# Performance work log

Hardware: AMD Instinct MI355X
Metric: run time of the kernel (lower is better)

Reference implementation:

```python
import jax, jax.numpy as jnp
import numpy as np

N_NODES = 200000
N_EDGES = 2000000
B = 1024
SEQ = 1000
EMB = 128
VOC = 26  # num_features_xt + 1
BN_EPS = 1e-5


def setup_inputs() -> dict:
    key = jax.random.key(0)
    ks = jax.random.split(key, 40)
    f32 = jnp.float32
    def nrm(k, shp, s=0.05):
        return jax.random.normal(k, shp, dtype=f32) * s
    inp = {}
    inp['x'] = jax.random.normal(ks[0], (N_NODES, 78), dtype=f32)
    inp['edge_index'] = jax.random.randint(ks[1], (2, N_EDGES), 0, N_NODES, dtype=jnp.int32)
    inp['batch'] = jnp.sort(jax.random.randint(ks[2], (N_NODES,), 0, B, dtype=jnp.int32))
    inp['target'] = jax.random.randint(ks[3], (B, SEQ), 0, VOC, dtype=jnp.int32)
    # GIN layer 1 (78 -> 32 -> 32)
    inp['W1a'] = nrm(ks[4], (78, 32)); inp['b1a'] = jnp.zeros((32,), f32)
    inp['W2a'] = nrm(ks[5], (32, 32)); inp['b2a'] = jnp.zeros((32,), f32)
    inp['g1'] = jnp.ones((32,), f32); inp['be1'] = jnp.zeros((32,), f32)
    # GIN layers 2-5 stacked
    inp['Ws1'] = nrm(ks[6], (4, 32, 32)); inp['bs1'] = jnp.zeros((4, 32), f32)
    inp['Ws2'] = nrm(ks[7], (4, 32, 32)); inp['bs2'] = jnp.zeros((4, 32), f32)
    inp['gs'] = jnp.ones((4, 32), f32); inp['bes'] = jnp.zeros((4, 32), f32)
    # drug head
    inp['fc1xd_W'] = nrm(ks[8], (32, 128)); inp['fc1xd_b'] = jnp.zeros((128,), f32)
    # protein branch
    inp['emb'] = nrm(ks[9], (VOC, EMB), 1.0)
    inp['convW'] = nrm(ks[10], (32, SEQ, 8))  # Conv1d(1000, 32, k=8): (O, I, K)
    inp['convb'] = jnp.zeros((32,), f32)
    inp['fcxt_W'] = nrm(ks[11], (32 * 121, 128)); inp['fcxt_b'] = jnp.zeros((128,), f32)
    # joint head
    inp['fc1_W'] = nrm(ks[12], (256, 1024)); inp['fc1_b'] = jnp.zeros((1024,), f32)
    inp['fc2_W'] = nrm(ks[13], (1024, 256)); inp['fc2_b'] = jnp.zeros((256,), f32)
    inp['out_W'] = nrm(ks[14], (256, 1)); inp['out_b'] = jnp.zeros((1,), f32)
    return inp


def _bn(h, g, b):
    m = h.mean(axis=0)
    v = h.var(axis=0)
    return (h - m) * jax.lax.rsqrt(v + BN_EPS) * g + b


def _gin(x, src, dst, W1, b1, W2, b2):
    # GIN aggregation (eps=0): (1+eps)*x + sum_{j->i} x_j, then 2-layer MLP
    agg = jax.ops.segment_sum(x[src], dst, num_segments=x.shape[0]) + x
    return jnp.maximum(agg @ W1 + b1, 0.0) @ W2 + b2


def reference(x, edge_index, batch, target, W1a, b1a, W2a, b2a, g1, be1,
              Ws1, bs1, Ws2, bs2, gs, bes, fc1xd_W, fc1xd_b, emb, convW, convb,
              fcxt_W, fcxt_b, fc1_W, fc1_b, fc2_W, fc2_b, out_W, out_b):
    relu = jax.nn.relu
    src, dst = edge_index[0], edge_index[1]
    h = _bn(relu(_gin(x, src, dst, W1a, b1a, W2a, b2a)), g1, be1)
    for i in range(4):
        h = _bn(relu(_gin(h, src, dst, Ws1[i], bs1[i], Ws2[i], bs2[i])), gs[i], bes[i])
    nb = target.shape[0]
    pooled = jax.ops.segment_sum(h, batch, num_segments=nb)  # [B, 32]
    xd = relu(pooled @ fc1xd_W + fc1xd_b)  # dropout: identity at eval
    # protein branch: embedding [B, 1000, 128] -> Conv1d over C=1000, L=128
    xe = emb[target]
    conv = jax.lax.conv_general_dilated(xe, convW, (1,), 'VALID',
                                        dimension_numbers=('NCH', 'OIH', 'NCH'))
    conv = conv + convb[None, :, None]  # [B, 32, 121]
    xt = conv.reshape(nb, 32 * 121) @ fcxt_W + fcxt_b
    xc = jnp.concatenate([xd, xt], axis=1)
    xc = relu(xc @ fc1_W + fc1_b)
    xc = relu(xc @ fc2_W + fc2_b)
    return xc @ out_W + out_b
```

## Files before the change

### kernel.cpp

```cpp
#include <hip/hip_runtime.h>

#define N_NODES 200000
#define N_EDGES 2000000
#define BATCH   1024
#define SEQ     1000
#define EMBD    128
#define VOC     26
#define BN_EPS  1e-5f
#define NB      128
#define NBUK    1563
#define CAP     2048
#define STG     8192
#define BPT     7



__global__ __launch_bounds__(256, 1) void k_bscatter(const int* __restrict__ ei,
                                                     int* __restrict__ gcnt,
                                                     unsigned int* __restrict__ epk) {
    __shared__ int lcnt[NBUK];
    __shared__ int lpos[NBUK];
    __shared__ int sbase[NBUK];
    __shared__ int ssum[256];
    __shared__ int2 stage[STG];
    int tid = threadIdx.x;
    int e0 = blockIdx.x * STG;
    int m = min(STG, N_EDGES - e0);
    for (int i = tid; i < NBUK; i += 256) lcnt[i] = 0;
    __syncthreads();
    for (int i = tid; i < m; i += 256) {
        int d = ei[N_EDGES + e0 + i];
        atomicAdd(&lcnt[d >> 7], 1);
    }
    __syncthreads();
    int v[BPT]; int s0 = 0; int bb = tid * BPT;
#pragma unroll
    for (int k = 0; k < BPT; k++) {
        int idx = bb + k;
        v[k] = (idx < NBUK) ? lcnt[idx] : 0;
        s0 += v[k];
    }
    ssum[tid] = s0;
    __syncthreads();
    for (int off = 1; off < 256; off <<= 1) {
        int x = (tid >= off) ? ssum[tid - off] : 0;
        __syncthreads();
        ssum[tid] += x;
        __syncthreads();
    }
    int run = ssum[tid] - s0;
#pragma unroll
    for (int k = 0; k < BPT; k++) {
        int idx = bb + k;
        if (idx < NBUK) { lpos[idx] = run; run += v[k]; }
    }
    __syncthreads();
    for (int i = tid; i < NBUK; i += 256) {
        int c = lcnt[i];
        if (c > 0) {
            int gb = atomicAdd(&gcnt[i], c);
            sbase[i] = gb - lpos[i];
        }
    }
    __syncthreads();
    for (int i = tid; i < m; i += 256) {
        int s = ei[e0 + i];
        int d = ei[N_EDGES + e0 + i];
        int p = atomicAdd(&lpos[d >> 7], 1);
        stage[p] = make_int2(s, d);
    }
    __syncthreads();
    for (int i = tid; i < m; i += 256) {
        int2 ed = stage[i];
        int b = ed.y >> 7;
        int slot = sbase[b] + i;
        if (slot < CAP)
            epk[(size_t)b * CAP + slot] = ((unsigned int)ed.x << 8) | (unsigned int)(ed.y & 127);
    }
}

__global__ __launch_bounds__(256, 8) void k_bsort(const int* __restrict__ gcnt,
                                                  unsigned int* __restrict__ epk,
                                                  int* __restrict__ deg) {
    __shared__ unsigned int stg[CAP];
    __shared__ unsigned int srt[CAP];
    __shared__ int cnt[NB];
    __shared__ int pos[NB];
    int b = blockIdx.x, tid = threadIdx.x;
    int fill = min(gcnt[b], CAP);
    unsigned int* slab = epk + (size_t)b * CAP;
    for (int i = tid; i < fill; i += 256) stg[i] = slab[i];
    if (tid < NB) cnt[tid] = 0;
    __syncthreads();
    for (int i = tid; i < fill; i += 256) atomicAdd(&cnt[stg[i] & (NB - 1)], 1);
    __syncthreads();
    if (tid < NB) { pos[tid] = cnt[tid]; deg[b * NB + tid] = cnt[tid]; }
    __syncthreads();
    for (int off = 1; off < NB; off <<= 1) {
        int x = (tid < NB && tid >= off) ? pos[tid - off] : 0;
        __syncthreads();
        if (tid < NB) pos[tid] += x;
        __syncthreads();
    }
    if (tid < NB) cnt[tid] = pos[tid] - cnt[tid];
    __syncthreads();
    for (int i = tid; i < fill; i += 256) {
        int p = atomicAdd(&cnt[stg[i] & (NB - 1)], 1);
        srt[p] = stg[i];
    }
    __syncthreads();
    for (int i = tid; i < fill; i += 256) slab[i] = srt[i];
}


__global__ __launch_bounds__(128) void k_proj78(const float* __restrict__ x,
                                                const float* __restrict__ W,
                                                float* __restrict__ y) {
    __shared__ __align__(16) float xs[128 * 78];
    __shared__ __align__(16) float ws[78 * 32];
    int tid = threadIdx.x;
    int base = blockIdx.x * 128;
    for (int i = tid; i < 78 * 32; i += 128) ws[i] = W[i];
    int cnt = min(128, N_NODES - base);
    for (int i = tid; i < cnt * 78; i += 128) xs[i] = x[(size_t)base * 78 + i];
    __syncthreads();
    int n = base + tid;
    if (tid >= cnt) return;
    float acc[32];
#pragma unroll
    for (int j = 0; j < 32; j++) acc[j] = 0.f;
    const float* xr = &xs[tid * 78];
    for (int c = 0; c < 78; c++) {
        float xv = xr[c];
        const float4* w4 = (const float4*)&ws[c * 32];
#pragma unroll
        for (int j4 = 0; j4 < 8; j4++) {
            float4 w = w4[j4];
            acc[j4 * 4 + 0] += xv * w.x; acc[j4 * 4 + 1] += xv * w.y;
            acc[j4 * 4 + 2] += xv * w.z; acc[j4 * 4 + 3] += xv * w.w;
        }
    }
    float4* yo = (float4*)&y[(size_t)n * 32];
#pragma unroll
    for (int j4 = 0; j4 < 8; j4++)
        yo[j4] = make_float4(acc[j4*4], acc[j4*4+1], acc[j4*4+2], acc[j4*4+3]);
}

template <bool FOLD>
__global__ __launch_bounds__(256, 4) void k_gmlp(const float* __restrict__ hin,
                                                 const int* __restrict__ gcnt,
                                                 const unsigned int* __restrict__ epk,
                                                 const int* __restrict__ deg,
                                                 const float* __restrict__ stats,
                                                 const float* __restrict__ g,
                                                 const float* __restrict__ be,
                                                 const float* __restrict__ W1,
                                                 const float* __restrict__ b1,
                                                 const float* __restrict__ W2,
                                                 const float* __restrict__ b2,
                                                 float* __restrict__ h,
                                                 float* __restrict__ statsOut) {
    __shared__ __align__(16) float ts[NB * 33];
    __shared__ __align__(16) float w2s[1024];
    __shared__ __align__(16) float wc[FOLD ? 1024 : 4];
    __shared__ __align__(16) unsigned int es[CAP];
    __shared__ float as_[FOLD ? 32 : 1], cs_[FOLD ? 32 : 1], cv[FOLD ? 32 : 1];
    __shared__ float b1s[32], b2s[32];
    __shared__ float sp[8][32], sq[8][32];
    int tid = threadIdx.x, base = blockIdx.x * NB;
    for (int i = tid; i < 1024; i += 256) w2s[i] = W2[i];
    if (tid < 32) { b1s[tid] = b1[tid]; b2s[tid] = b2[tid]; }
    if constexpr (FOLD) {
        if (tid < 32) {
            float inv_n = 1.f / (float)N_NODES;
            float m = stats[tid] * inv_n;
            float var = stats[32 + tid] * inv_n - m * m;
            float a = g[tid] * rsqrtf(var + BN_EPS);
            as_[tid] = a;
            cs_[tid] = be[tid] - m * a;
        }
        __syncthreads();
        for (int i = tid; i < 1024; i += 256) wc[i] = as_[i >> 5] * W1[i];
        if (tid < 32) {
            float s = 0.f;
            for (int k = 0; k < 32; k++) s += cs_[k] * W1[k * 32 + tid];
            cv[tid] = s;
        }
    }
    int cnt = min(NB, N_NODES - base);
    int fill = min(gcnt[blockIdx.x], CAP);
    int pfill = (fill + 255) & ~255;
    int dg = 0;
    if (FOLD && tid < cnt) dg = deg[base + tid];
    for (int i = tid; i < fill; i += 256) es[i] = epk[(size_t)blockIdx.x * CAP + i];
    for (int i = fill + tid; i < pfill; i += 256) es[i] = 128u;
    for (int i = tid; i < cnt * 32; i += 256) ts[(i >> 5) * 33 + (i & 31)] = hin[(size_t)base * 32 + i];
    __syncthreads();
    {
        int hw = tid >> 5, c = tid & 31;
        for (int se = hw * 32; se < pfill; se += 256) {
            float rr[32]; unsigned int dpk[8];
#pragma unroll
            for (int k4 = 0; k4 < 8; k4++) {
                unsigned int dp = 0;
#pragma unroll
                for (int q = 0; q < 4; q++) {
                    unsigned int p = es[se + k4 * 4 + q];
                    rr[k4 * 4 + q] = hin[(size_t)(p >> 8) * 32 + c];
                    dp |= (p & 255u) << (8 * q);
                }
                dpk[k4] = dp;
            }
            float acc = rr[0]; int cur = (int)(dpk[0] & 255u);
#pragma unroll
            for (int k = 1; k < 32; k++) {
                int d = (int)((dpk[k >> 2] >> (8 * (k & 3))) & 255u);
                if (d == cur) acc += rr[k];
                else { atomicAdd(&ts[cur * 33 + c], acc); acc = rr[k]; cur = d; }
            }
            if (cur < 128) atomicAdd(&ts[cur * 33 + c], acc);
        }
    }
    __syncthreads();
    float t[32];
    if (tid < cnt) {
        float v[32];
        if constexpr (FOLD) {
            float dgf = (float)(dg + 1);
#pragma unroll
            for (int j = 0; j < 32; j++) v[j] = b1s[j] + dgf * cv[j];
            for (int c = 0; c < 32; c++) {
                float av = ts[tid * 33 + c];
                const float4* w4 = (const float4*)&wc[c * 32];
#pragma unroll
                for (int j4 = 0; j4 < 8; j4++) {
                    float4 w = w4[j4];
                    v[j4*4+0] += av * w.x; v[j4*4+1] += av * w.y;
                    v[j4*4+2] += av * w.z; v[j4*4+3] += av * w.w;
                }
            }
        } else {
#pragma unroll
            for (int c = 0; c < 32; c++) v[c] = ts[tid * 33 + c] + b1s[c];
        }
        float acc[32];
#pragma unroll
        for (int j = 0; j < 32; j++) acc[j] = b2s[j];
        for (int c = 0; c < 32; c++) {
            float zv = fmaxf(v[c], 0.f);
            const float4* w4 = (const float4*)&w2s[c * 32];
#pragma unroll
            for (int j4 = 0; j4 < 8; j4++) {
                float4 w = w4[j4];
                acc[j4*4+0] += zv * w.x; acc[j4*4+1] += zv * w.y;
                acc[j4*4+2] += zv * w.z; acc[j4*4+3] += zv * w.w;
            }
        }
#pragma unroll
        for (int j = 0; j < 32; j++) t[j] = fmaxf(acc[j], 0.f);
    } else {
#pragma unroll
        for (int j = 0; j < 32; j++) t[j] = 0.f;
    }
    __syncthreads();
    if (tid < NB) {
#pragma unroll
        for (int c = 0; c < 32; c++) ts[tid * 33 + c] = t[c];
    }
    __syncthreads();
    {
        int c = tid & 31, gg = tid >> 5;
        float s = 0.f, q = 0.f;
        for (int r = gg * 16; r < gg * 16 + 16; r++) { float vv = ts[r * 33 + c]; s += vv; q += vv * vv; }
        sp[gg][c] = s; sq[gg][c] = q;
    }
    __syncthreads();
    if (tid < 32) {
        float s = 0.f, q = 0.f;
#pragma unroll
        for (int gg = 0; gg < 8; gg++) { s += sp[gg][tid]; q += sq[gg][tid]; }
        atomicAdd(&statsOut[tid], s);
        atomicAdd(&statsOut[32 + tid], q);
    }
    for (int i = tid; i < cnt * 32; i += 256) h[(size_t)base * 32 + i] = ts[(i >> 5) * 33 + (i & 31)];
}

__device__ __forceinline__ int lbound(const int* __restrict__ b, int val) {
    int lo = 0, hi = N_NODES;
    while (lo < hi) { int mid = (lo + hi) >> 1; if (b[mid] < val) lo = mid + 1; else hi = mid; }
    return lo;
}

__global__ __launch_bounds__(256) void k_pool(const float* __restrict__ h,
                                              const int* __restrict__ batch,
                                              const float* __restrict__ stats,
                                              const float* __restrict__ gw,
                                              const float* __restrict__ be,
                                              float* __restrict__ pooled) {
    __shared__ float sp[8][32];
    int g = blockIdx.x;
    int start = lbound(batch, g), end = lbound(batch, g + 1);
    int c = threadIdx.x & 31, gg = threadIdx.x >> 5;
    float acc = 0.f;
    for (int r = start + gg; r < end; r += 8) acc += h[(size_t)r * 32 + c];
    sp[gg][c] = acc;
    __syncthreads();
    if (threadIdx.x < 32) {
        int j = threadIdx.x;
        float s = 0.f;
#pragma unroll
        for (int k = 0; k < 8; k++) s += sp[k][j];
        float inv_n = 1.f / (float)N_NODES;
        float m = stats[j] * inv_n;
        float var = stats[32 + j] * inv_n - m * m;
        float a = gw[j] * rsqrtf(var + BN_EPS);
        float cc = be[j] - m * a;
        pooled[g * 32 + j] = a * s + cc * (float)(end - start);
    }
}

__global__ __launch_bounds__(256) void k_xd(const float* __restrict__ pooled,
                                            const float* __restrict__ W,
                                            const float* __restrict__ b,
                                            float* __restrict__ xc) {
    int t = blockIdx.x * 256 + threadIdx.x;
    int row = t >> 7, col = t & 127;
    if (row >= BATCH) return;
    float acc = b[col];
    for (int k = 0; k < 32; k++) acc += pooled[row * 32 + k] * W[k * 128 + col];
    xc[row * 256 + col] = fmaxf(acc, 0.f);
}


__global__ __launch_bounds__(256) void k_trw(const float* __restrict__ convW,
                                             float* __restrict__ Wt) {
    int t = blockIdx.x * 256 + threadIdx.x;
    if (t >= 32 * SEQ * 8) return;
    int o = t / (SEQ * 8), r = t % (SEQ * 8), i = r >> 3, k = r & 7;
    Wt[i * 256 + o * 8 + k] = convW[t];
}

__global__ __launch_bounds__(256) void k_prot1(const int* __restrict__ target,
                                               const float* __restrict__ Wt,
                                               float* __restrict__ Sg) {
    __shared__ int tv[SEQ];
    __shared__ int pos_[SEQ];
    __shared__ int off_[VOC + 1];
    __shared__ int cur_[VOC];
    int tid = threadIdx.x, b = blockIdx.x;
    for (int i = tid; i < SEQ; i += 256) tv[i] = target[(size_t)b * SEQ + i];
    if (tid < VOC + 1) off_[tid] = 0;
    __syncthreads();
    for (int i = tid; i < SEQ; i += 256) atomicAdd(&off_[tv[i] + 1], 1);
    __syncthreads();
    if (tid == 0) for (int v = 1; v <= VOC; v++) off_[v] += off_[v - 1];
    __syncthreads();
    if (tid < VOC) cur_[tid] = off_[tid];
    __syncthreads();
    for (int i = tid; i < SEQ; i += 256) {
        int p = atomicAdd(&cur_[tv[i]], 1);
        pos_[p] = i;
    }
    __syncthreads();
    for (int v = 0; v < VOC; v++) {
        int e0 = off_[v], e1 = off_[v + 1];
        float a0 = 0.f, a1 = 0.f, a2 = 0.f, a3 = 0.f, a4 = 0.f, a5 = 0.f, a6 = 0.f, a7 = 0.f;
        int k = e0;
        for (; k + 8 <= e1; k += 8) {
            a0 += Wt[(size_t)pos_[k + 0] * 256 + tid];
            a1 += Wt[(size_t)pos_[k + 1] * 256 + tid];
            a2 += Wt[(size_t)pos_[k + 2] * 256 + tid];
            a3 += Wt[(size_t)pos_[k + 3] * 256 + tid];
            a4 += Wt[(size_t)pos_[k + 4] * 256 + tid];
            a5 += Wt[(size_t)pos_[k + 5] * 256 + tid];
            a6 += Wt[(size_t)pos_[k + 6] * 256 + tid];
            a7 += Wt[(size_t)pos_[k + 7] * 256 + tid];
        }
        for (; k < e1; k++) a0 += Wt[(size_t)pos_[k] * 256 + tid];
        Sg[((size_t)b * VOC + v) * 256 + tid] = ((a0 + a1) + (a2 + a3)) + ((a4 + a5) + (a6 + a7));
    }
}

__global__ __launch_bounds__(256, 4) void k_prot2(const float* __restrict__ Sg,
                                                  const float* __restrict__ emb,
                                                  const float* __restrict__ convb,
                                                  float* __restrict__ conv) {
    __shared__ __align__(16) float S[VOC * 256];
    __shared__ __align__(16) float embs[VOC * EMBD];
    int tid = threadIdx.x, b = blockIdx.x;
    for (int i = tid; i < VOC * 256; i += 256) S[i] = Sg[(size_t)b * (VOC * 256) + i];
    for (int i = tid; i < VOC * EMBD; i += 256) embs[i] = emb[i];
    __syncthreads();
    int og = tid >> 6, lt = tid & 63;
    bool has2 = (lt < 57);
    float acc0[8], acc1[8];
#pragma unroll
    for (int oi = 0; oi < 8; oi++) {
        float bb = convb[og * 8 + oi];
        acc0[oi] = bb; acc1[oi] = bb;
    }
    for (int v = 0; v < VOC; v++) {
        float er0[8], er1[8];
#pragma unroll
        for (int k = 0; k < 8; k++) er0[k] = embs[v * EMBD + lt + k];
#pragma unroll
        for (int k = 0; k < 8; k++) er1[k] = has2 ? embs[v * EMBD + lt + 64 + k] : 0.f;
        const float* sv = &S[v * 256 + og * 64];
#pragma unroll
        for (int oi = 0; oi < 8; oi++) {
#pragma unroll
            for (int k = 0; k < 8; k++) {
                float s = sv[oi * 8 + k];
                acc0[oi] += s * er0[k];
                acc1[oi] += s * er1[k];
            }
        }
    }
#pragma unroll
    for (int oi = 0; oi < 8; oi++) {
        int o = og * 8 + oi;
        conv[((size_t)b * 32 + o) * 121 + lt] = acc0[oi];
        if (has2) conv[((size_t)b * 32 + o) * 121 + lt + 64] = acc1[oi];
    }
}


__global__ __launch_bounds__(256) void k_init_bias(float* __restrict__ C, int ldc, int coff,
                                                   const float* __restrict__ bias, int nb) {
    int t = blockIdx.x * 256 + threadIdx.x;
    int row = t / nb, col = t % nb;
    if (row >= BATCH) return;
    C[row * ldc + coff + col] = bias[col];
}

template <int ROWS, bool ATOMIC, bool RELU>
__global__ __launch_bounds__(256, 3) void k_gemm(const float* __restrict__ A, int lda,
                                                 const float* __restrict__ W, int ldw,
                                                 const float* __restrict__ bias,
                                                 float* __restrict__ C, int ldc, int coff,
                                                 int mtc, int ntc, int klen) {
    constexpr int P  = ROWS + 4;
    constexpr int HR = ROWS / 2;
    constexpr int TPR = 256 / ROWS;
    __shared__ __align__(16) float As[64 * P];
    __shared__ __align__(16) float Ws[64 * 128];
    int bid = blockIdx.x;
    int mt = bid % mtc, nt = (bid / mtc) % ntc, ks = bid / (mtc * ntc);
    int row0 = mt * ROWS, col0 = nt * 128, k0 = ks * klen;
    int tid = threadIdx.x;
    int j = tid & 127, rh = tid >> 7;
    float acc[HR];
#pragma unroll
    for (int m = 0; m < HR; m++) acc[m] = (ATOMIC || bias == nullptr) ? 0.f : bias[col0 + j];
    int lr = tid / TPR, lk = tid % TPR;
    for (int kc = 0; kc < klen; kc += 64) {
        int cc = min(64, klen - kc);
        __syncthreads();
        for (int kk = lk; kk < cc; kk += TPR)
            As[kk * P + lr] = A[(size_t)(row0 + lr) * lda + k0 + kc + kk];
        for (int i = tid; i < cc * 32; i += 256) {
            int r = i >> 5, c4 = (i & 31) << 2;
            *(float4*)&Ws[r * 128 + c4] =
                *(const float4*)&W[(size_t)(k0 + kc + r) * ldw + col0 + c4];
        }
        __syncthreads();
#pragma unroll 4
        for (int kk = 0; kk < cc; kk++) {
            float w = Ws[kk * 128 + j];
            const float4* a4 = (const float4*)&As[kk * P + rh * HR];
#pragma unroll
            for (int m4 = 0; m4 < HR / 4; m4++) {
                float4 a = a4[m4];
                acc[m4*4+0] += a.x * w; acc[m4*4+1] += a.y * w;
                acc[m4*4+2] += a.z * w; acc[m4*4+3] += a.w * w;
            }
        }
    }
#pragma unroll
    for (int m = 0; m < HR; m++) {
        int row = row0 + rh * HR + m;
        float* p = &C[(size_t)row * ldc + coff + col0 + j];
        if (ATOMIC) atomicAdd(p, acc[m]);
        else { float v = acc[m]; if (RELU) v = fmaxf(v, 0.f); *p = v; }
    }
}

__global__ __launch_bounds__(256) void k_out(const float* __restrict__ xc2,
                                             const float* __restrict__ W,
                                             const float* __restrict__ b,
                                             float* __restrict__ out) {
    int gt = blockIdx.x * 256 + threadIdx.x;
    int wid = gt >> 6, lane = gt & 63;
    if (wid >= BATCH) return;
    float4 xv = ((const float4*)&xc2[(size_t)wid * 256])[lane];
    float4 wv = ((const float4*)W)[lane];
    float s = fmaxf(xv.x, 0.f) * wv.x + fmaxf(xv.y, 0.f) * wv.y +
              fmaxf(xv.z, 0.f) * wv.z + fmaxf(xv.w, 0.f) * wv.w;
    for (int off = 32; off; off >>= 1) s += __shfl_down(s, off, 64);
    if (lane == 0) out[wid] = s + b[0];
}


extern "C" void kernel_launch(void* const* d_in, const int* in_sizes, int n_in,
                              void* d_out, int out_size, void* d_ws, size_t ws_size,
                              hipStream_t stream) {
    const float* x      = (const float*)d_in[0];
    const int*   ei     = (const int*)d_in[1];
    const int*   batch  = (const int*)d_in[2];
    const int*   target = (const int*)d_in[3];
    const float* W1a = (const float*)d_in[4];
    const float* b1a = (const float*)d_in[5];
    const float* W2a = (const float*)d_in[6];
    const float* b2a = (const float*)d_in[7];
    const float* g1  = (const float*)d_in[8];
    const float* be1 = (const float*)d_in[9];
    const float* Ws1 = (const float*)d_in[10];
    const float* bs1 = (const float*)d_in[11];
    const float* Ws2 = (const float*)d_in[12];
    const float* bs2 = (const float*)d_in[13];
    const float* gs  = (const float*)d_in[14];
    const float* bes = (const float*)d_in[15];
    const float* fc1xd_W = (const float*)d_in[16];
    const float* fc1xd_b = (const float*)d_in[17];
    const float* emb   = (const float*)d_in[18];
    const float* convW = (const float*)d_in[19];
    const float* convb = (const float*)d_in[20];
    const float* fcxt_W = (const float*)d_in[21];
    const float* fcxt_b = (const float*)d_in[22];
    const float* fc1_W = (const float*)d_in[23];
    const float* fc1_b = (const float*)d_in[24];
    const float* fc2_W = (const float*)d_in[25];
    const float* fc2_b = (const float*)d_in[26];
    const float* out_W = (const float*)d_in[27];
    const float* out_b = (const float*)d_in[28];
    float* out = (float*)d_out;

    char* ws = (char*)d_ws;
    size_t off = 0;
    auto alloc = [&](size_t bytes) { char* p = ws + off; off += (bytes + 4095) & ~(size_t)4095; return p; };
    float* y    = (float*)alloc((size_t)N_NODES * 32 * 4);
    float* h    = (float*)alloc((size_t)N_NODES * 32 * 4);
    unsigned int* epk = (unsigned int*)alloc((size_t)NBUK * CAP * 4);
    int* gcnt = (int*)alloc((size_t)NBUK * 4);
    float* stats  = (float*)alloc(5 * 64 * 4);
    float* pooled = (float*)alloc(BATCH * 32 * 4);
    float* xc  = (float*)alloc(BATCH * 256 * 4);
    float* xc1 = (float*)alloc(BATCH * 1024 * 4);
    float* xc2 = (float*)alloc(BATCH * 256 * 4);
    float* Wt  = (float*)alloc(SEQ * 256 * 4);
    int* deg  = (int*)alloc((size_t)NBUK * NB * 4);
    float* Sg   = h;
    float* conv = y;

    hipMemsetAsync(stats, 0, 5 * 64 * 4, stream);
    hipMemsetAsync(gcnt, 0, (size_t)NBUK * 4, stream);

    const int PROJ78_G = (N_NODES + 127) / 128;
    const int PART_G   = (N_EDGES + STG - 1) / STG;

    k_bscatter<<<PART_G, 256, 0, stream>>>(ei, gcnt, epk);
    k_bsort<<<NBUK, 256, 0, stream>>>(gcnt, epk, deg);

    k_proj78<<<PROJ78_G, 128, 0, stream>>>(x, W1a, y);
    k_gmlp<false><<<NBUK, 256, 0, stream>>>(y, gcnt, epk, deg, nullptr, nullptr, nullptr,
                                            nullptr, b1a, W2a, b2a, h, stats);
    float* hin = h; float* hout = y;
    for (int i = 0; i < 4; i++) {
        const float* gg = (i == 0) ? g1 : gs + (i - 1) * 32;
        const float* bb = (i == 0) ? be1 : bes + (i - 1) * 32;
        k_gmlp<true><<<NBUK, 256, 0, stream>>>(hin, gcnt, epk, deg, stats + i * 64, gg, bb,
                                               Ws1 + i * 1024, bs1 + i * 32, Ws2 + i * 1024,
                                               bs2 + i * 32, hout, stats + (i + 1) * 64);
        float* tmp = hin; hin = hout; hout = tmp;
    }
    k_pool<<<BATCH, 256, 0, stream>>>(hin, batch, stats + 4 * 64, gs + 3 * 32, bes + 3 * 32, pooled);
    k_xd<<<(BATCH * 128) / 256, 256, 0, stream>>>(pooled, fc1xd_W, fc1xd_b, xc);
    k_trw<<<(32 * SEQ * 8) / 256, 256, 0, stream>>>(convW, Wt);
    k_prot1<<<BATCH, 256, 0, stream>>>(target, Wt, Sg);
    k_prot2<<<BATCH, 256, 0, stream>>>(Sg, emb, convb, conv);
    k_init_bias<<<(BATCH * 128) / 256, 256, 0, stream>>>(xc, 256, 128, fcxt_b, 128);
    k_gemm<32, true, false><<<32 * 1 * 16, 256, 0, stream>>>(conv, 3872, fcxt_W, 128, nullptr,
                                                             xc, 256, 128, 32, 1, 242);
    k_gemm<32, false, true><<<32 * 8 * 1, 256, 0, stream>>>(xc, 256, fc1_W, 1024, fc1_b,
                                                            xc1, 1024, 0, 32, 8, 256);
    k_init_bias<<<(BATCH * 256) / 256, 256, 0, stream>>>(xc2, 256, 0, fc2_b, 256);
    k_gemm<32, true, false><<<32 * 2 * 4, 256, 0, stream>>>(xc1, 1024, fc2_W, 256, nullptr,
                                                            xc2, 256, 0, 32, 2, 256);
    k_out<<<(BATCH * 64) / 256, 256, 0, stream>>>(xc2, out_W, out_b, out);
}
```

Measured before the change: 1.062 ms.

## Sort edges by source bucket, shrink bucket capacity, alias LDS to raise GIN occupancy

Edges within each destination bucket are now sorted by the high bits of the source index (p>>18) rather than by destination, so the gather from hin is more local; per-destination degree is still counted separately. Since destinations are no longer grouped, the segmented run-length accumulation is replaced by plain LDS atomics per edge with 16-edge batches. Bucket capacity shrinks, and the folded weight matrix and stat partials reuse the edge staging buffer after aggregation, cutting LDS so launch bounds can rise from 4 to 5 blocks per CU. The risks are more LDS atomics per edge and silent edge drops if a bucket exceeds the smaller capacity.

```diff
diff --git a/kernel.cpp b/kernel.cpp
--- a/kernel.cpp
+++ b/kernel.cpp
@@ -9,7 +9,7 @@
 #define BN_EPS  1e-5f
 #define NB      128
 #define NBUK    1563
-#define CAP     2048
+#define CAP     1664
 #define STG     8192
 #define BPT     7
 
@@ -84,28 +84,34 @@
                                                   int* __restrict__ deg) {
     __shared__ unsigned int stg[CAP];
     __shared__ unsigned int srt[CAP];
-    __shared__ int cnt[NB];
-    __shared__ int pos[NB];
+    __shared__ int cnt[256];
+    __shared__ int pos[256];
+    __shared__ int dcnt[NB];
     int b = blockIdx.x, tid = threadIdx.x;
     int fill = min(gcnt[b], CAP);
     unsigned int* slab = epk + (size_t)b * CAP;
     for (int i = tid; i < fill; i += 256) stg[i] = slab[i];
-    if (tid < NB) cnt[tid] = 0;
-    __syncthreads();
-    for (int i = tid; i < fill; i += 256) atomicAdd(&cnt[stg[i] & (NB - 1)], 1);
-    __syncthreads();
-    if (tid < NB) { pos[tid] = cnt[tid]; deg[b * NB + tid] = cnt[tid]; }
-    __syncthreads();
-    for (int off = 1; off < NB; off <<= 1) {
-        int x = (tid < NB && tid >= off) ? pos[tid - off] : 0;
-        __syncthreads();
-        if (tid < NB) pos[tid] += x;
-        __syncthreads();
-    }
-    if (tid < NB) cnt[tid] = pos[tid] - cnt[tid];
+    cnt[tid] = 0;
+    if (tid < NB) dcnt[tid] = 0;
     __syncthreads();
     for (int i = tid; i < fill; i += 256) {
-        int p = atomicAdd(&cnt[stg[i] & (NB - 1)], 1);
+        atomicAdd(&cnt[stg[i] >> 18], 1);
+        atomicAdd(&dcnt[stg[i] & (NB - 1)], 1);
+    }
+    __syncthreads();
+    pos[tid] = cnt[tid];
+    __syncthreads();
+    for (int off = 1; off < 256; off <<= 1) {
+        int x = (tid >= off) ? pos[tid - off] : 0;
+        __syncthreads();
+        pos[tid] += x;
+        __syncthreads();
+    }
+    cnt[tid] = pos[tid] - cnt[tid];
+    if (tid < NB) deg[b * NB + tid] = dcnt[tid];
+    __syncthreads();
+    for (int i = tid; i < fill; i += 256) {
+        int p = atomicAdd(&cnt[stg[i] >> 18], 1);
         srt[p] = stg[i];
     }
     __syncthreads();
@@ -147,7 +153,7 @@
 }
 
 template <bool FOLD>
-__global__ __launch_bounds__(256, 4) void k_gmlp(const float* __restrict__ hin,
+__global__ __launch_bounds__(256, 5) void k_gmlp(const float* __restrict__ hin,
                                                  const int* __restrict__ gcnt,
                                                  const unsigned int* __restrict__ epk,
                                                  const int* __restrict__ deg,
@@ -160,16 +166,41 @@
                                                  const float* __restrict__ b2,
                                                  float* __restrict__ h,
                                                  float* __restrict__ statsOut) {
-    __shared__ __align__(16) float ts[NB * 33];
+    __shared__ __align__(16) float ts[129 * 33];
     __shared__ __align__(16) float w2s[1024];
-    __shared__ __align__(16) float wc[FOLD ? 1024 : 4];
     __shared__ __align__(16) unsigned int es[CAP];
-    __shared__ float as_[FOLD ? 32 : 1], cs_[FOLD ? 32 : 1], cv[FOLD ? 32 : 1];
-    __shared__ float b1s[32], b2s[32];
-    __shared__ float sp[8][32], sq[8][32];
+    __shared__ float b1s[32], b2s[32], as_[32], cs_[32], cv[32];
     int tid = threadIdx.x, base = blockIdx.x * NB;
     for (int i = tid; i < 1024; i += 256) w2s[i] = W2[i];
     if (tid < 32) { b1s[tid] = b1[tid]; b2s[tid] = b2[tid]; }
+    int cnt = min(NB, N_NODES - base);
+    int fill = min(gcnt[blockIdx.x], CAP);
+    int pfill = (fill + 127) & ~127;
+    int dg = 0;
+    if (FOLD && tid < cnt) dg = deg[base + tid];
+    for (int i = tid; i < fill; i += 256) es[i] = epk[(size_t)blockIdx.x * CAP + i];
+    for (int i = fill + tid; i < pfill; i += 256) es[i] = 128u;
+    for (int i = tid; i < cnt * 32; i += 256) ts[(i >> 5) * 33 + (i & 31)] = hin[(size_t)base * 32 + i];
+    __syncthreads();
+    {
+        int hw = tid >> 5, c = tid & 31;
+        for (int se = hw * 16; se < pfill; se += 128) {
+            float rr[16];
+#pragma unroll
+            for (int k = 0; k < 16; k++) {
+                unsigned int p = es[se + k];
+                rr[k] = hin[(size_t)(p >> 8) * 32 + c];
+            }
+#pragma unroll
+            for (int k = 0; k < 16; k++) {
+                unsigned int p = es[se + k];
+                atomicAdd(&ts[(p & 255u) * 33 + c], rr[k]);
+            }
+        }
+    }
+    __syncthreads();
+    float* wc  = (float*)es;
+    float* spq = ((float*)es) + 1024;
     if constexpr (FOLD) {
         if (tid < 32) {
             float inv_n = 1.f / (float)N_NODES;
@@ -186,42 +217,8 @@
             for (int k = 0; k < 32; k++) s += cs_[k] * W1[k * 32 + tid];
             cv[tid] = s;
         }
-    }
-    int cnt = min(NB, N_NODES - base);
-    int fill = min(gcnt[blockIdx.x], CAP);
-    int pfill = (fill + 255) & ~255;
-    int dg = 0;
-    if (FOLD && tid < cnt) dg = deg[base + tid];
-    for (int i = tid; i < fill; i += 256) es[i] = epk[(size_t)blockIdx.x * CAP + i];
-    for (int i = fill + tid; i < pfill; i += 256) es[i] = 128u;
-    for (int i = tid; i < cnt * 32; i += 256) ts[(i >> 5) * 33 + (i & 31)] = hin[(size_t)base * 32 + i];
-    __syncthreads();
-    {
-        int hw = tid >> 5, c = tid & 31;
-        for (int se = hw * 32; se < pfill; se += 256) {
-            float rr[32]; unsigned int dpk[8];
-#pragma unroll
-            for (int k4 = 0; k4 < 8; k4++) {
-                unsigned int dp = 0;
-#pragma unroll
-                for (int q = 0; q < 4; q++) {
-                    unsigned int p = es[se + k4 * 4 + q];
-                    rr[k4 * 4 + q] = hin[(size_t)(p >> 8) * 32 + c];
-                    dp |= (p & 255u) << (8 * q);
-                }
-                dpk[k4] = dp;
-            }
-            float acc = rr[0]; int cur = (int)(dpk[0] & 255u);
-#pragma unroll
-            for (int k = 1; k < 32; k++) {
-                int d = (int)((dpk[k >> 2] >> (8 * (k & 3))) & 255u);
-                if (d == cur) acc += rr[k];
-                else { atomicAdd(&ts[cur * 33 + c], acc); acc = rr[k]; cur = d; }
-            }
-            if (cur < 128) atomicAdd(&ts[cur * 33 + c], acc);
-        }
-    }
-    __syncthreads();
+        __syncthreads();
+    }
     float t[32];
     if (tid < cnt) {
         float v[32];
@@ -272,13 +269,13 @@
         int c = tid & 31, gg = tid >> 5;
         float s = 0.f, q = 0.f;
         for (int r = gg * 16; r < gg * 16 + 16; r++) { float vv = ts[r * 33 + c]; s += vv; q += vv * vv; }
-        sp[gg][c] = s; sq[gg][c] = q;
+        spq[gg * 32 + c] = s; spq[256 + gg * 32 + c] = q;
     }
     __syncthreads();
     if (tid < 32) {
         float s = 0.f, q = 0.f;
 #pragma unroll
-        for (int gg = 0; gg < 8; gg++) { s += sp[gg][tid]; q += sq[gg][tid]; }
+        for (int gg = 0; gg < 8; gg++) { s += spq[gg * 32 + tid]; q += spq[256 + gg * 32 + tid]; }
         atomicAdd(&statsOut[tid], s);
         atomicAdd(&statsOut[32 + tid], q);
     }
```

Result: slower. 3.005 ms (+182.9%).
